# Performance work log

Hardware: AMD Instinct MI355X
Metric: run time of the kernel (lower is better)

Reference implementation:

```python
import jax, jax.numpy as jnp
import numpy as np

N = 4096        # nodes (atoms)
E = 65536       # edges (avg degree 16)
H = 128         # hidden_channels
R = 32          # num_rbf
MAX_Z = 128
CUTOFF_UPPER = 4.5
LN_EPS = 1e-5


def _linear_params(key, out_f, in_f, bias=True, scale=None):
    kw, kb = jax.random.split(key)
    s = scale if scale is not None else (1.0 / np.sqrt(in_f))
    W = jax.random.uniform(kw, (out_f, in_f), jnp.float32, -s, s)
    if bias:
        b = jax.random.uniform(kb, (out_f,), jnp.float32, -s, s)
        return W, b
    return W


def setup_inputs() -> dict:
    key = jax.random.key(0)
    ks = jax.random.split(key, 24)
    z = jax.random.randint(ks[0], (N,), 0, MAX_Z)
    edge_index = jax.random.randint(ks[1], (2, E), 0, N)
    edge_weight = jax.random.uniform(ks[2], (E,), jnp.float32) * CUTOFF_UPPER
    ev = jax.random.normal(ks[3], (E, 3), jnp.float32)
    edge_vec_norm = ev / jnp.linalg.norm(ev, axis=-1, keepdims=True)
    edge_attr = jax.random.uniform(ks[4], (E, R), jnp.float32)
    labels = jax.random.normal(ks[5], (N,), jnp.float32)
    labels_mask = jax.random.randint(ks[6], (N,), 0, 2).astype(bool)

    emb_w = jax.random.normal(ks[7], (MAX_Z, H), jnp.float32)  # nn.Embedding default N(0,1)
    emb2_w, emb2_b = _linear_params(ks[8], H, 2 * H)
    label_emb_w, label_emb_b = _linear_params(ks[9], H, 1)
    label_emb2_w, label_emb2_b = _linear_params(ks[10], H, 2 * H)
    mask_token = jax.random.normal(ks[11], (H,), jnp.float32)
    dp1_w, dp1_b = _linear_params(ks[12], H, R)
    dp2_w, dp2_b = _linear_params(ks[13], H, R)
    dp3_w, dp3_b = _linear_params(ks[14], H, R)
    lt0_w = _linear_params(ks[15], H, H, bias=False)
    lt1_w = _linear_params(ks[16], H, H, bias=False)
    lt2_w = _linear_params(ks[17], H, H, bias=False)
    ls1_w, ls1_b = _linear_params(ks[18], 2 * H, H)
    ls2_w, ls2_b = _linear_params(ks[19], 3 * H, 2 * H)
    ln_g = jnp.ones((H,), jnp.float32)
    ln_b = jnp.zeros((H,), jnp.float32)

    return dict(z=z, edge_index=edge_index, edge_weight=edge_weight,
                edge_vec_norm=edge_vec_norm, edge_attr=edge_attr,
                labels=labels, labels_mask=labels_mask,
                emb_w=emb_w, emb2_w=emb2_w, emb2_b=emb2_b,
                label_emb_w=label_emb_w, label_emb_b=label_emb_b,
                mask_token=mask_token,
                label_emb2_w=label_emb2_w, label_emb2_b=label_emb2_b,
                dp1_w=dp1_w, dp1_b=dp1_b, dp2_w=dp2_w, dp2_b=dp2_b,
                dp3_w=dp3_w, dp3_b=dp3_b,
                lt0_w=lt0_w, lt1_w=lt1_w, lt2_w=lt2_w,
                ls1_w=ls1_w, ls1_b=ls1_b, ls2_w=ls2_w, ls2_b=ls2_b,
                ln_g=ln_g, ln_b=ln_b)


def _cosine_cutoff(d):
    # cutoff_lower == 0 branch of CosineCutoff
    c = 0.5 * (jnp.cos(d * (np.pi / CUTOFF_UPPER)) + 1.0)
    return c * (d < CUTOFF_UPPER).astype(d.dtype)


def _skewtensor(v):
    zero = jnp.zeros_like(v[:, 0])
    t = jnp.stack([zero, -v[:, 2], v[:, 1],
                   v[:, 2], zero, -v[:, 0],
                   -v[:, 1], v[:, 0], zero], axis=1)
    return t.reshape(-1, 3, 3)


def _symtensor(v):
    vv = v[:, :, None] * v[:, None, :]               # [E,3,3], symmetric
    tr = jnp.trace(vv, axis1=-2, axis2=-1) / 3.0     # mean of diagonal
    eye = jnp.eye(3, dtype=v.dtype)
    return vv - tr[:, None, None] * eye              # traceless symmetric part


def _layernorm(x, g, b):
    mu = jnp.mean(x, axis=-1, keepdims=True)
    var = jnp.mean(jnp.square(x - mu), axis=-1, keepdims=True)
    return (x - mu) * jax.lax.rsqrt(var + LN_EPS) * g + b


def reference(z, edge_index, edge_weight, edge_vec_norm, edge_attr, labels,
              labels_mask, emb_w, emb2_w, emb2_b, label_emb_w, label_emb_b,
              mask_token, label_emb2_w, label_emb2_b, dp1_w, dp1_b, dp2_w,
              dp2_b, dp3_w, dp3_b, lt0_w, lt1_w, lt2_w, ls1_w, ls1_b, ls2_w,
              ls2_b, ln_g, ln_b):
    src, dst = edge_index[0], edge_index[1]
    n = z.shape[0]

    # --- atomic-number message: Zij = emb2(concat(Z[src], Z[dst])) ---
    Z = emb_w[z]                                                   # [N,H]
    Zij = jnp.concatenate([Z[src], Z[dst]], -1) @ emb2_w.T + emb2_b  # [E,H]

    # --- label message with mask-token substitution ---
    L = labels[:, None] @ label_emb_w.T + label_emb_b              # [N,H]
    L = jnp.where(labels_mask[:, None], mask_token, L)
    Lij = jnp.concatenate([L[src], L[dst]], -1) @ label_emb2_w.T + label_emb2_b

    # --- tensor messages ---
    CZ = _cosine_cutoff(edge_weight)[:, None] * (Zij + Lij)        # [E,H]
    eye = jnp.eye(3, dtype=edge_vec_norm.dtype)
    f1 = edge_attr @ dp1_w.T + dp1_b                               # [E,H]
    f2 = edge_attr @ dp2_w.T + dp2_b
    f3 = edge_attr @ dp3_w.T + dp3_b
    skew = _skewtensor(edge_vec_norm)                              # [E,3,3]
    sym = _symtensor(edge_vec_norm)                                # [E,3,3]
    Iij = (f1 * CZ)[:, :, None, None] * eye                        # [E,H,3,3]
    Aij = (f2 * CZ)[:, :, None, None] * skew[:, None]
    Sij = (f3 * CZ)[:, :, None, None] * sym[:, None]

    # --- scatter-add into node tensors ---
    I = jax.ops.segment_sum(Iij, src, num_segments=n)              # [N,H,3,3]
    A = jax.ops.segment_sum(Aij, src, num_segments=n)
    S = jax.ops.segment_sum(Sij, src, num_segments=n)

    # --- norm + scalar MLP gating ---
    X3 = I + A + S
    norm = jnp.sum(jnp.square(X3), axis=(-2, -1))                  # tensor_norm -> [N,H]
    norm = _layernorm(norm, ln_g, ln_b)
    norm = jax.nn.silu(norm @ ls1_w.T + ls1_b)                     # [N,2H]
    norm = jax.nn.silu(norm @ ls2_w.T + ls2_b)                     # [N,3H]
    norm = norm.reshape(n, -1, 3)                                  # [N,H,3]

    # --- channel-mixing linears over hidden dim, gated per component ---
    I = jnp.einsum('nhij,gh->ngij', I, lt0_w) * norm[:, :, 0, None, None]
    A = jnp.einsum('nhij,gh->ngij', A, lt1_w) * norm[:, :, 1, None, None]
    S = jnp.einsum('nhij,gh->ngij', S, lt2_w) * norm[:, :, 2, None, None]
    return I + A + S                                               # [N,H,3,3]
```

## Files before the change

### kernel.cpp

```cpp
#include <hip/hip_runtime.h>
#include <hip/hip_bf16.h>
#include <math.h>

#define NN 4096
#define EE 65536
#define HH 128
#define RR 32
#define MAXZ 128
#define CUT 4.5f
#define PI_OVER_CUT 0.6981317007977318f
#define LN_EPS 1e-5f

typedef unsigned short u16;
typedef unsigned int u32;
typedef unsigned char u8;
typedef _Float16 h2 __attribute__((ext_vector_type(2)));
typedef _Float16 hf8 __attribute__((ext_vector_type(8)));
typedef float f32x4 __attribute__((ext_vector_type(4)));

__device__ __forceinline__ float dot4(float4 a, float4 b){
    return a.x*b.x + a.y*b.y + a.z*b.z + a.w*b.w;
}
__device__ __forceinline__ float silu(float x){ return x / (1.f + __expf(-x)); }
__device__ __forceinline__ u32 packh2(float a, float b){
    union{u32 u; h2 h;} v; v.h = (h2){(_Float16)a, (_Float16)b}; return v.u;
}
__device__ __forceinline__ float fdot2u(u32 a, u32 b, float c){
    union{u32 u; h2 h;} x, y; x.u = a; y.u = b;
    return __builtin_amdgcn_fdot2(x.h, y.h, c, false);
}
__device__ __forceinline__ u16 f2h(float f){
    union{u16 u; _Float16 h;} v; v.h = (_Float16)f; return v.u;
}
__device__ __forceinline__ float h2f(u16 u){
    union{u16 u_; _Float16 h;} v; v.u_ = u; return (float)v.h;
}

__global__ void k_sig(float* __restrict__ out, float val, int n){
    int i = blockIdx.x*256 + threadIdx.x;
    if (i < n) out[i] = val;
}

__global__ void k_zero(int* __restrict__ deg){
    deg[blockIdx.x*256 + threadIdx.x] = 0;
}

__global__ __launch_bounds__(256) void k_cvt(const u8* __restrict__ zr,
                                             const u8* __restrict__ eir,
                                             const u8* __restrict__ mr,
                                             int* __restrict__ z32,
                                             int* __restrict__ ei32,
                                             int* __restrict__ m32,
                                             int* __restrict__ deg){
    __shared__ int sF1, sF3, sOdd, sZ64, sE64;
    int t = threadIdx.x;
    if (t == 0){ sF1=0; sF3=0; sOdd=0; sZ64=1; sE64=1; }
    __syncthreads();
    for (int i = t; i < 4096; i += 256){
        u8 b = mr[i];
        if ((i & 3) == 1 && b == 0x3F) sF1 = 1;
        if ((i & 3) == 3 && b == 0x3F) sF3 = 1;
        if ((i & 3) != 0 && b != 0)    sOdd = 1;
    }
    const u32* zw = (const u32*)zr;
    const u32* ew = (const u32*)eir;
    for (int i = t; i < 128; i += 256) if (zw[2*i + 1]) sZ64 = 0;
    for (int i = t; i < 512; i += 256) if (ew[2*i + 1]) sE64 = 0;
    __syncthreads();
    int mf = sF1 ? 2 : (sF3 ? 0 : (sOdd ? 1 : 0));
    int z64 = sZ64, e64 = sE64;

    int i = blockIdx.x*256 + t;
    if (i < NN){
        z32[i] = z64 ? ((const int*)zr)[2*i] : ((const int*)zr)[i];
        int mm;
        if (mf == 1)      mm = (mr[i] != 0);
        else if (mf == 2) mm = (((const u16*)mr)[i] != 0);
        else              mm = (((const u32*)mr)[i] != 0u);
        m32[i] = mm;
    }
    if (i < 2*EE){
        int v = e64 ? ((const int*)eir)[2*i] : ((const int*)eir)[i];
        ei32[i] = v;
        if (i < EE) atomicAdd(&deg[v], 1);
    }
}

__global__ __launch_bounds__(256) void k_scan(const int* __restrict__ deg,
                                              int* __restrict__ offsets,
                                              int* __restrict__ cursor){
    int t = threadIdx.x;
    int lane = t & 63, wid = t >> 6;
    int4 d[4];
    #pragma unroll
    for (int q = 0; q < 4; ++q) d[q] = ((const int4*)deg)[t*4 + q];
    int vals[16];
    #pragma unroll
    for (int q = 0; q < 4; ++q){
        vals[4*q+0]=d[q].x; vals[4*q+1]=d[q].y; vals[4*q+2]=d[q].z; vals[4*q+3]=d[q].w;
    }
    int sum = 0;
    #pragma unroll
    for (int q = 0; q < 16; ++q) sum += vals[q];
    int incl = sum;
    #pragma unroll
    for (int dd = 1; dd < 64; dd <<= 1){ int s = __shfl_up(incl, dd); if (lane >= dd) incl += s; }
    __shared__ int wsum[4];
    if (lane == 63) wsum[wid] = incl;
    __syncthreads();
    int base = 0;
    for (int w = 0; w < wid; ++w) base += wsum[w];
    int run = base + incl - sum;
    #pragma unroll
    for (int q = 0; q < 16; ++q){
        offsets[t*16 + q] = run;
        cursor [t*16 + q] = run;
        run += vals[q];
    }
    if (t == 255) offsets[NN] = run;
}

__global__ __launch_bounds__(256) void k_semeta(
    const int* __restrict__ ei, int* __restrict__ cursor,
    const float* __restrict__ ew, const float* __restrict__ ev,
    const float* __restrict__ ea,
    u32* __restrict__ attrSh, int* __restrict__ dstA, float4* __restrict__ metaA)
{
    int e = blockIdx.x*256 + threadIdx.x;
    if (e >= EE) return;
    int s = ei[e];
    int p = atomicAdd(&cursor[s], 1);
    float d = ew[e];
    float cutv = (d < CUT) ? 0.5f*(__cosf(d*PI_OVER_CUT) + 1.f) : 0.f;
    dstA[p] = ei[EE + e];
    metaA[p] = make_float4(cutv, ev[3*e], ev[3*e+1], ev[3*e+2]);
    const float* a = ea + (size_t)e*RR;
    u32* o = attrSh + (size_t)p*16;
    #pragma unroll
    for (int q = 0; q < 16; ++q)
        o[q] = packh2(cutv*a[2*q], cutv*a[2*q+1]);
}

__global__ __launch_bounds__(256) void k_prep(
    const float* __restrict__ ls1_w, const float* __restrict__ ls2_w,
    const float* __restrict__ lt0_w, const float* __restrict__ lt1_w,
    const float* __restrict__ lt2_w,
    const float* __restrict__ dp1_w, const float* __restrict__ dp2_w,
    const float* __restrict__ dp3_w,
    const float* __restrict__ emb_w, const float* __restrict__ emb2_w,
    const float* __restrict__ label_emb_w, const float* __restrict__ label_emb_b,
    const float* __restrict__ mask_token, const float* __restrict__ label_emb2_w,
    const float* __restrict__ label_emb2_b, const float* __restrict__ emb2_b,
    u16* __restrict__ ls1H, u16* __restrict__ ls2H, u16* __restrict__ ltH,
    u32* __restrict__ dpTh, float* __restrict__ PzA, float* __restrict__ PzB,
    float* __restrict__ vecs)
{
    int b = blockIdx.x, t = threadIdx.x;
    if (b < 728){
        int i = b*256 + t;
        if (i < 32768){ ls1H[i] = f2h(ls1_w[i]); return; }
        i -= 32768;
        if (i < 98304){ ls2H[i] = f2h(ls2_w[i]); return; }
        i -= 98304;
        if (i < 16384){ ltH[0*16384 + i] = f2h(lt0_w[i]); return; }
        i -= 16384;
        if (i < 16384){ ltH[1*16384 + i] = f2h(lt1_w[i]); return; }
        i -= 16384;
        if (i < 16384){ ltH[2*16384 + i] = f2h(lt2_w[i]); return; }
        i -= 16384;
        if (i < 6144){
            int j = i >> 11, rem = i & 2047, q = rem >> 7, h = rem & 127;
            const float* src = (j == 0) ? dp1_w : ((j == 1) ? dp2_w : dp3_w);
            dpTh[(j*16 + q)*HH + h] = packh2(src[h*RR + 2*q], src[h*RR + 2*q + 1]);
            return;
        }
        return;
    }
    if (b < 792){
        int zi = (b - 728)*2 + (t >> 7), h = t & 127;
        __shared__ float Zs[2][HH];
        Zs[t >> 7][h] = emb_w[zi*HH + h];
        __syncthreads();
        const float4* wa = (const float4*)(emb2_w + h*2*HH);
        const float4* wb = (const float4*)(emb2_w + h*2*HH + HH);
        float pa = 0.f, pb = 0.f;
        const float* Z = Zs[t >> 7];
        #pragma unroll 8
        for (int j = 0; j < HH/4; ++j){
            float4 zp = *(const float4*)&Z[4*j];
            pa += dot4(wa[j], zp);
            pb += dot4(wb[j], zp);
        }
        PzA[zi*HH + h] = pa;
        PzB[zi*HH + h] = pb;
        return;
    }
    if (t < 128){
        int h = t;
        const float* wa = label_emb2_w + h*2*HH;
        const float* wb = wa + HH;
        float uA=0.f,vA=0.f,wA=0.f,uB=0.f,vB=0.f,wB=0.f;
        for (int j = 0; j < HH; ++j){
            float a = wa[j], bb = wb[j];
            float u = label_emb_w[j], v = label_emb_b[j], m = mask_token[j];
            uA += a*u; vA += a*v; wA += a*m;
            uB += bb*u; vB += bb*v; wB += bb*m;
        }
        float bias = emb2_b[h] + label_emb2_b[h];
        vecs[0*HH + h] = uA;
        vecs[1*HH + h] = vA + bias;
        vecs[2*HH + h] = wA + bias;
        vecs[3*HH + h] = uB;
        vecs[4*HH + h] = vB;
        vecs[5*HH + h] = wB;
    }
}

__global__ __launch_bounds__(256) void k_comb(const int* __restrict__ z32,
                                              const int* __restrict__ m32,
                                              const float* __restrict__ labels,
                                              const float* __restrict__ PzA,
                                              const float* __restrict__ PzB,
                                              const float* __restrict__ vecs,
                                              float* __restrict__ Pa,
                                              u16* __restrict__ Pbh)
{
    int i = blockIdx.x*256 + threadIdx.x;
    int n = i >> 7, h = i & 127;
    int zi = z32[n];
    int mk = m32[n];
    float lab = labels[n];
    float la = mk ? vecs[2*HH + h] : lab*vecs[0*HH + h] + vecs[1*HH + h];
    float lb = mk ? vecs[5*HH + h] : lab*vecs[3*HH + h] + vecs[4*HH + h];
    Pa[i]  = PzA[zi*HH + h] + la;
    Pbh[i] = f2h(PzB[zi*HH + h] + lb);
}

__global__ __launch_bounds__(128) void k_gather(
    const u32* __restrict__ attrSh, const int* __restrict__ dstA,
    const float4* __restrict__ metaA,
    const u32* __restrict__ dpTh,
    const float* __restrict__ dp1_b, const float* __restrict__ dp2_b,
    const float* __restrict__ dp3_b,
    const float* __restrict__ Pa, const u16* __restrict__ Pbh,
    const int* __restrict__ offsets,
    u16* __restrict__ X0, u16* __restrict__ X1, u16* __restrict__ X2,
    float* __restrict__ norm2)
{
    int n = blockIdx.x, t = threadIdx.x;
    u32 w1[16], w2[16], w3[16];
    #pragma unroll
    for (int q = 0; q < 16; ++q){
        w1[q] = dpTh[(0*16 + q)*HH + t];
        w2[q] = dpTh[(1*16 + q)*HH + t];
        w3[q] = dpTh[(2*16 + q)*HH + t];
    }
    float fb1 = dp1_b[t], fb2 = dp2_b[t], fb3 = dp3_b[t];
    float pa = Pa[n*HH + t];
    float ai = 0.f, aw0 = 0.f, aw1 = 0.f, aw2 = 0.f;
    float m00 = 0.f, m01 = 0.f, m02 = 0.f, m11 = 0.f, m12 = 0.f, m22 = 0.f;

    int e0 = offsets[n], e1 = offsets[n+1];
    int j = e0;
    for (; j + 1 < e1; j += 2){
        int dsta = dstA[j], dstb = dstA[j+1];
        float4 ma = metaA[j], mb = metaA[j+1];
        float sa = pa + h2f(Pbh[(size_t)dsta*HH + t]);
        float sb = pa + h2f(Pbh[(size_t)dstb*HH + t]);
        const u32* Aa = attrSh + (size_t)j*16;
        const u32* Ab = Aa + 16;
        float f1a = ma.x*fb1, f2a = ma.x*fb2, f3a = ma.x*fb3;
        float f1b = mb.x*fb1, f2b = mb.x*fb2, f3b = mb.x*fb3;
        #pragma unroll
        for (int q = 0; q < 16; ++q){
            u32 a = Aa[q], bq = Ab[q];
            f1a = fdot2u(a, w1[q], f1a);
            f2a = fdot2u(a, w2[q], f2a);
            f3a = fdot2u(a, w3[q], f3a);
            f1b = fdot2u(bq, w1[q], f1b);
            f2b = fdot2u(bq, w2[q], f2b);
            f3b = fdot2u(bq, w3[q], f3b);
        }
        float aa = f1a*sa, ba = f2a*sa, ca = f3a*sa;
        float ab = f1b*sb, bb = f2b*sb, cb = f3b*sb;
        ai  += aa;            ai  += ab;
        aw0 += ba*ma.y;       aw0 += bb*mb.y;
        aw1 += ba*ma.z;       aw1 += bb*mb.z;
        aw2 += ba*ma.w;       aw2 += bb*mb.w;
        float cva0 = ca*ma.y, cva1 = ca*ma.z;
        float cvb0 = cb*mb.y, cvb1 = cb*mb.z;
        m00 += cva0*ma.y;     m00 += cvb0*mb.y;
        m01 += cva0*ma.z;     m01 += cvb0*mb.z;
        m02 += cva0*ma.w;     m02 += cvb0*mb.w;
        m11 += cva1*ma.z;     m11 += cvb1*mb.z;
        m12 += cva1*ma.w;     m12 += cvb1*mb.w;
        m22 += ca*ma.w*ma.w;  m22 += cb*mb.w*mb.w;
    }
    if (j < e1){
        int dst = dstA[j];
        float4 m4 = metaA[j];
        float s = pa + h2f(Pbh[(size_t)dst*HH + t]);
        const u32* Aa = attrSh + (size_t)j*16;
        float f1 = m4.x*fb1, f2 = m4.x*fb2, f3 = m4.x*fb3;
        #pragma unroll
        for (int q = 0; q < 16; ++q){
            u32 a = Aa[q];
            f1 = fdot2u(a, w1[q], f1);
            f2 = fdot2u(a, w2[q], f2);
            f3 = fdot2u(a, w3[q], f3);
        }
        float a = f1*s, b = f2*s, c = f3*s;
        ai  += a;
        aw0 += b*m4.y; aw1 += b*m4.z; aw2 += b*m4.w;
        float cv0 = c*m4.y, cv1 = c*m4.z;
        m00 += cv0*m4.y; m01 += cv0*m4.z; m02 += cv0*m4.w;
        m11 += cv1*m4.z; m12 += cv1*m4.w; m22 += c*m4.w*m4.w;
    }

    X0[(size_t)n*HH + t] = f2h(ai);
    u16* x1p = X1 + (size_t)3*n*HH + t;
    x1p[0*HH] = f2h(aw0); x1p[1*HH] = f2h(aw1); x1p[2*HH] = f2h(aw2);
    u16* x2p = X2 + (size_t)6*n*HH + t;
    x2p[0*HH] = f2h(m00); x2p[1*HH] = f2h(m01); x2p[2*HH] = f2h(m02);
    x2p[3*HH] = f2h(m11); x2p[4*HH] = f2h(m12); x2p[5*HH] = f2h(m22);

    float tr3 = (m00 + m11 + m22) * (1.f/3.f);
    float x00 = ai + m00 - tr3, x11 = ai + m11 - tr3, x22 = ai + m22 - tr3;
    float nn = x00*x00 + x11*x11 + x22*x22
             + 2.f*(m01*m01 + aw2*aw2 + m02*m02 + aw1*aw1 + m12*m12 + aw0*aw0);
    norm2[n*HH + t] = nn;
}

__global__ __launch_bounds__(256) void k_gatesM(
    const float* __restrict__ norm2, const float* __restrict__ ln_g,
    const float* __restrict__ ln_b,
    const u16* __restrict__ ls1H, const float* __restrict__ ls1_b,
    const u16* __restrict__ ls2H, const float* __restrict__ ls2_b,
    float* __restrict__ gates)
{
    int n0 = blockIdx.x * 16;
    int t = threadIdx.x;
    int wave = t >> 6, lane = t & 63;
    int rlo = lane & 15, kb = lane >> 4;
    __shared__ u16 ysH[16][136];
    __shared__ u16 usH[16][264];

    {
        int ni = wave*4 + kb;
        int n = n0 + ni;
        float x[8]; float s = 0.f;
        #pragma unroll
        for (int k = 0; k < 8; ++k){ x[k] = norm2[(size_t)n*HH + rlo + 16*k]; s += x[k]; }
        #pragma unroll
        for (int d = 1; d < 16; d <<= 1) s += __shfl_xor(s, d);
        float mu = s * (1.f/HH);
        float q = 0.f;
        #pragma unroll
        for (int k = 0; k < 8; ++k){ float dx = x[k]-mu; q += dx*dx; }
        #pragma unroll
        for (int d = 1; d < 16; d <<= 1) q += __shfl_xor(q, d);
        float rs = rsqrtf(q*(1.f/HH) + LN_EPS);
        #pragma unroll
        for (int k = 0; k < 8; ++k){
            int h = rlo + 16*k;
            ysH[ni][h] = f2h((x[k]-mu)*rs*ln_g[h] + ln_b[h]);
        }
    }
    __syncthreads();

    {
        hf8 a[4];
        #pragma unroll
        for (int ks = 0; ks < 4; ++ks)
            a[ks] = *(const hf8*)&ysH[rlo][kb*8 + ks*32];
        for (int ct = wave; ct < 16; ct += 4){
            f32x4 acc = (f32x4){0.f,0.f,0.f,0.f};
            const u16* wr0 = ls1H + (size_t)(ct*16 + rlo)*HH;
            #pragma unroll
            for (int ks = 0; ks < 4; ++ks){
                hf8 bf = *(const hf8*)(wr0 + kb*8 + ks*32);
                acc = __builtin_amdgcn_mfma_f32_16x16x32_f16(a[ks], bf, acc, 0, 0, 0);
            }
            float bias = ls1_b[ct*16 + rlo];
            #pragma unroll
            for (int j = 0; j < 4; ++j)
                usH[kb*4 + j][ct*16 + rlo] = f2h(silu(acc[j] + bias));
        }
    }
    __syncthreads();

    {
        hf8 a[8];
        #pragma unroll
        for (int ks = 0; ks < 8; ++ks)
            a[ks] = *(const hf8*)&usH[rlo][kb*8 + ks*32];
        for (int ct = wave; ct < 24; ct += 4){
            f32x4 acc = (f32x4){0.f,0.f,0.f,0.f};
            const u16* wr0 = ls2H + (size_t)(ct*16 + rlo)*256;
            #pragma unroll
            for (int ks = 0; ks < 8; ++ks){
                hf8 bf = *(const hf8*)(wr0 + kb*8 + ks*32);
                acc = __builtin_amdgcn_mfma_f32_16x16x32_f16(a[ks], bf, acc, 0, 0, 0);
            }
            float bias = ls2_b[ct*16 + rlo];
            #pragma unroll
            for (int j = 0; j < 4; ++j){
                int n = n0 + kb*4 + j;
                gates[(size_t)n*384 + ct*16 + rlo] = silu(acc[j] + bias);
            }
        }
    }
}

__global__ __launch_bounds__(256) void k_gemmout(
    const u16* __restrict__ X0, const u16* __restrict__ X1, const u16* __restrict__ X2,
    const u16* __restrict__ ltH, const float* __restrict__ gates,
    float* __restrict__ out)
{
    int n0 = blockIdx.x * 16;
    int wave = threadIdx.x >> 6, lane = threadIdx.x & 63;
    int rlo = lane & 15, kb = lane >> 4;
    __shared__ u16 Yl[160*136];

    for (int tile = wave; tile < 10; tile += 4){
        const u16* X; const u16* W; int rbase;
        if (tile == 0)     { X = X0; W = ltH;         rbase = n0; }
        else if (tile < 4) { X = X1; W = ltH + 16384; rbase = 3*n0 + (tile-1)*16; }
        else               { X = X2; W = ltH + 32768; rbase = 6*n0 + (tile-4)*16; }

        const hf8* xr = (const hf8*)(X + (size_t)(rbase + rlo)*HH + kb*8);
        hf8 a[4];
        #pragma unroll
        for (int ks = 0; ks < 4; ++ks) a[ks] = xr[ks*4];

        #pragma unroll
        for (int ct = 0; ct < 8; ++ct){
            f32x4 acc = (f32x4){0.f,0.f,0.f,0.f};
            const hf8* wr = (const hf8*)(W + (size_t)(ct*16 + rlo)*HH + kb*8);
            #pragma unroll
            for (int ks = 0; ks < 4; ++ks)
                acc = __builtin_amdgcn_mfma_f32_16x16x32_f16(a[ks], wr[ks*4], acc, 0, 0, 0);
            #pragma unroll
            for (int j = 0; j < 4; ++j)
                Yl[(tile*16 + kb*4 + j)*136 + ct*16 + rlo] = f2h(acc[j]);
        }
    }
    __syncthreads();

    #pragma unroll
    for (int q = 0; q < 8; ++q){
        int id = q*256 + threadIdx.x;
        int ni = id >> 7, g = id & 127;
        int n = n0 + ni;
        float mi  = h2f(Yl[ni*136 + g]);
        float mw0 = h2f(Yl[(16 + 3*ni + 0)*136 + g]);
        float mw1 = h2f(Yl[(16 + 3*ni + 1)*136 + g]);
        float mw2 = h2f(Yl[(16 + 3*ni + 2)*136 + g]);
        float mm0 = h2f(Yl[(64 + 6*ni + 0)*136 + g]);
        float mm1 = h2f(Yl[(64 + 6*ni + 1)*136 + g]);
        float mm2 = h2f(Yl[(64 + 6*ni + 2)*136 + g]);
        float mm3 = h2f(Yl[(64 + 6*ni + 3)*136 + g]);
        float mm4 = h2f(Yl[(64 + 6*ni + 4)*136 + g]);
        float mm5 = h2f(Yl[(64 + 6*ni + 5)*136 + g]);
        float g0 = gates[(size_t)n*384 + 3*g];
        float g1 = gates[(size_t)n*384 + 3*g + 1];
        float g2 = gates[(size_t)n*384 + 3*g + 2];
        float t3 = (mm0 + mm3 + mm5) * (1.f/3.f);
        float* op = out + ((size_t)n*HH + g)*9;
        op[0] =  g0*mi  + g2*(mm0 - t3);
        op[1] = -g1*mw2 + g2*mm1;
        op[2] =  g1*mw1 + g2*mm2;
        op[3] =  g1*mw2 + g2*mm1;
        op[4] =  g0*mi  + g2*(mm3 - t3);
        op[5] = -g1*mw0 + g2*mm4;
        op[6] = -g1*mw1 + g2*mm2;
        op[7] =  g1*mw0 + g2*mm4;
        op[8] =  g0*mi  + g2*(mm5 - t3);
    }
}

extern "C" void kernel_launch(void* const* d_in, const int* in_sizes, int n_in,
                              void* d_out, int out_size, void* d_ws, size_t ws_size,
                              hipStream_t stream)
{
    float* out = (float*)d_out;
    int sig_blocks = (out_size + 255)/256;

    if (out_size != NN*HH*9){
        k_sig<<<sig_blocks, 256, 0, stream>>>(out, 400.f, out_size);
        return;
    }
    if (n_in != 30){
        k_sig<<<sig_blocks, 256, 0, stream>>>(out, 300.f + (float)n_in, out_size);
        return;
    }
    static const int want[30] = {
        4096, 131072, 65536, 196608, 2097152, 4096, 4096,
        16384, 32768, 128, 128, 128, 128, 32768, 128,
        4096, 128, 4096, 128, 4096, 128,
        16384, 16384, 16384, 32768, 256, 98304, 384, 128, 128
    };
    for (int i = 0; i < 30; ++i){
        if (in_sizes[i] != want[i]){
            k_sig<<<sig_blocks, 256, 0, stream>>>(out, 200.f + (float)i, out_size);
            return;
        }
    }

    const u8*    z_raw        = (const u8*)d_in[0];
    const u8*    ei_raw       = (const u8*)d_in[1];
    const float* edge_weight  = (const float*)d_in[2];
    const float* edge_vec     = (const float*)d_in[3];
    const float* edge_attr    = (const float*)d_in[4];
    const float* labels       = (const float*)d_in[5];
    const u8*    mask_raw     = (const u8*)d_in[6];
    const float* emb_w        = (const float*)d_in[7];
    const float* emb2_w       = (const float*)d_in[8];
    const float* emb2_b       = (const float*)d_in[9];
    const float* label_emb_w  = (const float*)d_in[10];
    const float* label_emb_b  = (const float*)d_in[11];
    const float* mask_token   = (const float*)d_in[12];
    const float* label_emb2_w = (const float*)d_in[13];
    const float* label_emb2_b = (const float*)d_in[14];
    const float* dp1_w = (const float*)d_in[15];
    const float* dp1_b = (const float*)d_in[16];
    const float* dp2_w = (const float*)d_in[17];
    const float* dp2_b = (const float*)d_in[18];
    const float* dp3_w = (const float*)d_in[19];
    const float* dp3_b = (const float*)d_in[20];
    const float* lt0_w = (const float*)d_in[21];
    const float* lt1_w = (const float*)d_in[22];
    const float* lt2_w = (const float*)d_in[23];
    const float* ls1_w = (const float*)d_in[24];
    const float* ls1_b = (const float*)d_in[25];
    const float* ls2_w = (const float*)d_in[26];
    const float* ls2_b = (const float*)d_in[27];
    const float* ln_g  = (const float*)d_in[28];
    const float* ln_b  = (const float*)d_in[29];

    char* ws = (char*)d_ws;
    size_t off = 0;
    auto alloc = [&](size_t bytes) -> void* {
        void* p = ws + off;
        off += (bytes + 255) & ~(size_t)255;
        return p;
    };
    float* Pa      = (float*)alloc((size_t)NN*HH*4);
    u16*   Pbh     = (u16*)alloc((size_t)NN*HH*2);
    float* norm2   = (float*)alloc((size_t)NN*HH*4);
    float* gates   = (float*)alloc((size_t)NN*384*4);
    float* PzA     = (float*)alloc((size_t)MAXZ*HH*4);
    float* PzB     = (float*)alloc((size_t)MAXZ*HH*4);
    float* vecs    = (float*)alloc((size_t)6*HH*4);
    u32*   dpTh    = (u32*)alloc((size_t)3*16*HH*4);
    u16*   ls1H    = (u16*)alloc((size_t)32768*2);
    u16*   ls2H    = (u16*)alloc((size_t)98304*2);
    u16*   ltH     = (u16*)alloc((size_t)3*16384*2);
    u16*   X0      = (u16*)alloc((size_t)NN*HH*2);
    u16*   X1      = (u16*)alloc((size_t)3*NN*HH*2);
    u16*   X2      = (u16*)alloc((size_t)6*NN*HH*2);
    u32*   attrSh  = (u32*)alloc((size_t)EE*16*4);
    float* metaA   = (float*)alloc((size_t)EE*16);
    int*   dstA    = (int*)alloc((size_t)EE*4);
    int*   z32     = (int*)alloc((size_t)NN*4);
    int*   ei32    = (int*)alloc((size_t)2*EE*4);
    int*   m32     = (int*)alloc((size_t)NN*4);
    int*   deg     = (int*)alloc((size_t)NN*4);
    int*   offsets = (int*)alloc((size_t)(NN+1)*4);
    int*   cursor  = (int*)alloc((size_t)NN*4);

    if (off > ws_size){
        k_sig<<<sig_blocks, 256, 0, stream>>>(out, 150.f, out_size);
        return;
    }

    k_zero   <<<NN/256, 256, 0, stream>>>(deg);
    k_cvt    <<<(2*EE + 255)/256, 256, 0, stream>>>(z_raw, ei_raw, mask_raw,
                                                    z32, ei32, m32, deg);
    k_scan   <<<1, 256, 0, stream>>>(deg, offsets, cursor);
    k_semeta <<<EE/256, 256, 0, stream>>>(ei32, cursor, edge_weight, edge_vec,
                                          edge_attr, attrSh, dstA, (float4*)metaA);
    k_prep   <<<793, 256, 0, stream>>>(ls1_w, ls2_w, lt0_w, lt1_w, lt2_w,
                                       dp1_w, dp2_w, dp3_w,
                                       emb_w, emb2_w,
                                       label_emb_w, label_emb_b, mask_token,
                                       label_emb2_w, label_emb2_b, emb2_b,
                                       ls1H, ls2H, ltH, dpTh, PzA, PzB, vecs);
    k_comb   <<<NN*HH/256, 256, 0, stream>>>(z32, m32, labels, PzA, PzB, vecs, Pa, Pbh);
    k_gather <<<NN, 128, 0, stream>>>(attrSh, dstA, (const float4*)metaA,
                                      dpTh, dp1_b, dp2_b, dp3_b,
                                      Pa, Pbh, offsets, X0, X1, X2, norm2);
    k_gatesM <<<NN/16, 256, 0, stream>>>(norm2, ln_g, ln_b, ls1H, ls1_b,
                                         ls2H, ls2_b, gates);
    k_gemmout<<<256, 256, 0, stream>>>(X0, X1, X2, ltH, gates, out);
}
```

Baseline: 104.6 us.

## Merge front-end kernels with last-block scan, fuse edge/comb and gates/gemmout

Cuts the launch count from eight kernels to five. The convert, scan and weight-prep kernels become one launch, where the last block to finish (tracked by an atomic counter) runs the degree prefix scan. Edge sorting and node-embedding combination share one launch. The gates MLP and the output channel-mixing GEMM share a 512-thread block, with the X tiles prefetched before the MLP. The goal is less launch overhead and fewer idle gaps between small kernels, at the cost of a serialized last-block scan and higher per-block LDS and register use in the fused tail.

New measurement: 107.0 us. 1.02x slower.

```diff
diff --git a/kernel.cpp b/kernel.cpp
--- a/kernel.cpp
+++ b/kernel.cpp
@@ -41,107 +41,17 @@
     if (i < n) out[i] = val;
 }
 
-__global__ void k_zero(int* __restrict__ deg){
-    deg[blockIdx.x*256 + threadIdx.x] = 0;
-}
-
-__global__ __launch_bounds__(256) void k_cvt(const u8* __restrict__ zr,
-                                             const u8* __restrict__ eir,
-                                             const u8* __restrict__ mr,
-                                             int* __restrict__ z32,
-                                             int* __restrict__ ei32,
-                                             int* __restrict__ m32,
-                                             int* __restrict__ deg){
-    __shared__ int sF1, sF3, sOdd, sZ64, sE64;
-    int t = threadIdx.x;
-    if (t == 0){ sF1=0; sF3=0; sOdd=0; sZ64=1; sE64=1; }
-    __syncthreads();
-    for (int i = t; i < 4096; i += 256){
-        u8 b = mr[i];
-        if ((i & 3) == 1 && b == 0x3F) sF1 = 1;
-        if ((i & 3) == 3 && b == 0x3F) sF3 = 1;
-        if ((i & 3) != 0 && b != 0)    sOdd = 1;
-    }
-    const u32* zw = (const u32*)zr;
-    const u32* ew = (const u32*)eir;
-    for (int i = t; i < 128; i += 256) if (zw[2*i + 1]) sZ64 = 0;
-    for (int i = t; i < 512; i += 256) if (ew[2*i + 1]) sE64 = 0;
-    __syncthreads();
-    int mf = sF1 ? 2 : (sF3 ? 0 : (sOdd ? 1 : 0));
-    int z64 = sZ64, e64 = sE64;
-
-    int i = blockIdx.x*256 + t;
-    if (i < NN){
-        z32[i] = z64 ? ((const int*)zr)[2*i] : ((const int*)zr)[i];
-        int mm;
-        if (mf == 1)      mm = (mr[i] != 0);
-        else if (mf == 2) mm = (((const u16*)mr)[i] != 0);
-        else              mm = (((const u32*)mr)[i] != 0u);
-        m32[i] = mm;
-    }
-    if (i < 2*EE){
-        int v = e64 ? ((const int*)eir)[2*i] : ((const int*)eir)[i];
-        ei32[i] = v;
-        if (i < EE) atomicAdd(&deg[v], 1);
-    }
-}
-
-__global__ __launch_bounds__(256) void k_scan(const int* __restrict__ deg,
-                                              int* __restrict__ offsets,
-                                              int* __restrict__ cursor){
-    int t = threadIdx.x;
-    int lane = t & 63, wid = t >> 6;
-    int4 d[4];
-    #pragma unroll
-    for (int q = 0; q < 4; ++q) d[q] = ((const int4*)deg)[t*4 + q];
-    int vals[16];
-    #pragma unroll
-    for (int q = 0; q < 4; ++q){
-        vals[4*q+0]=d[q].x; vals[4*q+1]=d[q].y; vals[4*q+2]=d[q].z; vals[4*q+3]=d[q].w;
-    }
-    int sum = 0;
-    #pragma unroll
-    for (int q = 0; q < 16; ++q) sum += vals[q];
-    int incl = sum;
-    #pragma unroll
-    for (int dd = 1; dd < 64; dd <<= 1){ int s = __shfl_up(incl, dd); if (lane >= dd) incl += s; }
-    __shared__ int wsum[4];
-    if (lane == 63) wsum[wid] = incl;
-    __syncthreads();
-    int base = 0;
-    for (int w = 0; w < wid; ++w) base += wsum[w];
-    int run = base + incl - sum;
-    #pragma unroll
-    for (int q = 0; q < 16; ++q){
-        offsets[t*16 + q] = run;
-        cursor [t*16 + q] = run;
-        run += vals[q];
-    }
-    if (t == 255) offsets[NN] = run;
-}
-
-__global__ __launch_bounds__(256) void k_semeta(
-    const int* __restrict__ ei, int* __restrict__ cursor,
-    const float* __restrict__ ew, const float* __restrict__ ev,
-    const float* __restrict__ ea,
-    u32* __restrict__ attrSh, int* __restrict__ dstA, float4* __restrict__ metaA)
-{
-    int e = blockIdx.x*256 + threadIdx.x;
-    if (e >= EE) return;
-    int s = ei[e];
-    int p = atomicAdd(&cursor[s], 1);
-    float d = ew[e];
-    float cutv = (d < CUT) ? 0.5f*(__cosf(d*PI_OVER_CUT) + 1.f) : 0.f;
-    dstA[p] = ei[EE + e];
-    metaA[p] = make_float4(cutv, ev[3*e], ev[3*e+1], ev[3*e+2]);
-    const float* a = ea + (size_t)e*RR;
-    u32* o = attrSh + (size_t)p*16;
-    #pragma unroll
-    for (int q = 0; q < 16; ++q)
-        o[q] = packh2(cutv*a[2*q], cutv*a[2*q+1]);
-}
-
-__global__ __launch_bounds__(256) void k_prep(
+__global__ void k_zero(int* __restrict__ deg, int* __restrict__ doneCnt){
+    int i = blockIdx.x*256 + threadIdx.x;
+    deg[i] = 0;
+    if (i == 0) doneCnt[0] = 0;
+}
+
+__global__ __launch_bounds__(256) void k_front(
+    const u8* __restrict__ zr, const u8* __restrict__ eir, const u8* __restrict__ mr,
+    int* __restrict__ z32, int* __restrict__ ei32, int* __restrict__ m32,
+    int* __restrict__ deg, int* __restrict__ doneCnt,
+    int* __restrict__ offsets, int* __restrict__ cursor,
     const float* __restrict__ ls1_w, const float* __restrict__ ls2_w,
     const float* __restrict__ lt0_w, const float* __restrict__ lt1_w,
     const float* __restrict__ lt2_w,
@@ -156,8 +66,84 @@
     float* __restrict__ vecs)
 {
     int b = blockIdx.x, t = threadIdx.x;
-    if (b < 728){
+    if (b < 512){
+        __shared__ int sF1, sF3, sOdd, sZ64, sE64;
+        if (t == 0){ sF1=0; sF3=0; sOdd=0; sZ64=1; sE64=1; }
+        __syncthreads();
+        for (int i = t; i < 4096; i += 256){
+            u8 bb = mr[i];
+            if ((i & 3) == 1 && bb == 0x3F) sF1 = 1;
+            if ((i & 3) == 3 && bb == 0x3F) sF3 = 1;
+            if ((i & 3) != 0 && bb != 0)    sOdd = 1;
+        }
+        const u32* zw = (const u32*)zr;
+        const u32* ew = (const u32*)eir;
+        for (int i = t; i < 128; i += 256) if (zw[2*i + 1]) sZ64 = 0;
+        for (int i = t; i < 512; i += 256) if (ew[2*i + 1]) sE64 = 0;
+        __syncthreads();
+        int mf = sF1 ? 2 : (sF3 ? 0 : (sOdd ? 1 : 0));
+        int z64 = sZ64, e64 = sE64;
+
         int i = b*256 + t;
+        if (i < NN){
+            z32[i] = z64 ? ((const int*)zr)[2*i] : ((const int*)zr)[i];
+            int mm;
+            if (mf == 1)      mm = (mr[i] != 0);
+            else if (mf == 2) mm = (((const u16*)mr)[i] != 0);
+            else              mm = (((const u32*)mr)[i] != 0u);
+            m32[i] = mm;
+        }
+        if (i < 2*EE){
+            int v = e64 ? ((const int*)eir)[2*i] : ((const int*)eir)[i];
+            ei32[i] = v;
+            if (i < EE) atomicAdd(&deg[v], 1);
+        }
+
+        __syncthreads();
+        __shared__ int isLast;
+        if (t == 0){
+            __threadfence();
+            int old = __hip_atomic_fetch_add(doneCnt, 1, __ATOMIC_ACQ_REL,
+                                             __HIP_MEMORY_SCOPE_AGENT);
+            isLast = (old == 511);
+        }
+        __syncthreads();
+        if (isLast){
+            int lane = t & 63, wid = t >> 6;
+            int vals[16];
+            #pragma unroll
+            for (int q = 0; q < 16; ++q)
+                vals[q] = __hip_atomic_load(&deg[t*16 + q], __ATOMIC_RELAXED,
+                                            __HIP_MEMORY_SCOPE_AGENT);
+            int sum = 0;
+            #pragma unroll
+            for (int q = 0; q < 16; ++q) sum += vals[q];
+            int incl = sum;
+            #pragma unroll
+            for (int dd = 1; dd < 64; dd <<= 1){
+                int s2 = __shfl_up(incl, dd);
+                if (lane >= dd) incl += s2;
+            }
+            __shared__ int wsum[4];
+            if (lane == 63) wsum[wid] = incl;
+            __syncthreads();
+            int base = 0;
+            for (int w = 0; w < wid; ++w) base += wsum[w];
+            int run = base + incl - sum;
+            #pragma unroll
+            for (int q = 0; q < 16; ++q){
+                offsets[t*16 + q] = run;
+                cursor [t*16 + q] = run;
+                run += vals[q];
+            }
+            if (t == 255) offsets[NN] = run;
+        }
+        return;
+    }
+
+    int pb = b - 512;
+    if (pb < 728){
+        int i = pb*256 + t;
         if (i < 32768){ ls1H[i] = f2h(ls1_w[i]); return; }
         i -= 32768;
         if (i < 98304){ ls2H[i] = f2h(ls2_w[i]); return; }
@@ -176,23 +162,23 @@
         }
         return;
     }
-    if (b < 792){
-        int zi = (b - 728)*2 + (t >> 7), h = t & 127;
+    if (pb < 792){
+        int zi = (pb - 728)*2 + (t >> 7), h = t & 127;
         __shared__ float Zs[2][HH];
         Zs[t >> 7][h] = emb_w[zi*HH + h];
         __syncthreads();
         const float4* wa = (const float4*)(emb2_w + h*2*HH);
         const float4* wb = (const float4*)(emb2_w + h*2*HH + HH);
-        float pa = 0.f, pb = 0.f;
+        float pa = 0.f, pbv = 0.f;
         const float* Z = Zs[t >> 7];
         #pragma unroll 8
         for (int j = 0; j < HH/4; ++j){
             float4 zp = *(const float4*)&Z[4*j];
-            pa += dot4(wa[j], zp);
-            pb += dot4(wb[j], zp);
+            pa  += dot4(wa[j], zp);
+            pbv += dot4(wb[j], zp);
         }
         PzA[zi*HH + h] = pa;
-        PzB[zi*HH + h] = pb;
+        PzB[zi*HH + h] = pbv;
         return;
     }
     if (t < 128){
@@ -216,16 +202,34 @@
     }
 }
 
-__global__ __launch_bounds__(256) void k_comb(const int* __restrict__ z32,
-                                              const int* __restrict__ m32,
-                                              const float* __restrict__ labels,
-                                              const float* __restrict__ PzA,
-                                              const float* __restrict__ PzB,
-                                              const float* __restrict__ vecs,
-                                              float* __restrict__ Pa,
-                                              u16* __restrict__ Pbh)
+__global__ __launch_bounds__(256) void k_edge(
+    const int* __restrict__ ei, int* __restrict__ cursor,
+    const float* __restrict__ ew, const float* __restrict__ ev,
+    const float* __restrict__ ea,
+    u32* __restrict__ attrSh, int* __restrict__ dstA, float4* __restrict__ metaA,
+    const int* __restrict__ z32, const int* __restrict__ m32,
+    const float* __restrict__ labels,
+    const float* __restrict__ PzA, const float* __restrict__ PzB,
+    const float* __restrict__ vecs,
+    float* __restrict__ Pa, u16* __restrict__ Pbh)
 {
-    int i = blockIdx.x*256 + threadIdx.x;
+    int b = blockIdx.x, t = threadIdx.x;
+    if (b < 256){
+        int e = b*256 + t;
+        int s = ei[e];
+        int p = atomicAdd(&cursor[s], 1);
+        float d = ew[e];
+        float cutv = (d < CUT) ? 0.5f*(__cosf(d*PI_OVER_CUT) + 1.f) : 0.f;
+        dstA[p] = ei[EE + e];
+        metaA[p] = make_float4(cutv, ev[3*e], ev[3*e+1], ev[3*e+2]);
+        const float* a = ea + (size_t)e*RR;
+        u32* o = attrSh + (size_t)p*16;
+        #pragma unroll
+        for (int q = 0; q < 16; ++q)
+            o[q] = packh2(cutv*a[2*q], cutv*a[2*q+1]);
+        return;
+    }
+    int i = (b - 256)*256 + t;
     int n = i >> 7, h = i & 127;
     int zi = z32[n];
     int mk = m32[n];
@@ -309,9 +313,9 @@
             f2 = fdot2u(a, w2[q], f2);
             f3 = fdot2u(a, w3[q], f3);
         }
-        float a = f1*s, b = f2*s, c = f3*s;
+        float a = f1*s, bb = f2*s, c = f3*s;
         ai  += a;
-        aw0 += b*m4.y; aw1 += b*m4.z; aw2 += b*m4.w;
+        aw0 += bb*m4.y; aw1 += bb*m4.z; aw2 += bb*m4.w;
         float cv0 = c*m4.y, cv1 = c*m4.z;
         m00 += cv0*m4.y; m01 += cv0*m4.z; m02 += cv0*m4.w;
         m11 += cv1*m4.z; m12 += cv1*m4.w; m22 += c*m4.w*m4.w;
@@ -331,12 +335,15 @@
     norm2[n*HH + t] = nn;
 }
 
-__global__ __launch_bounds__(256) void k_gatesM(
+__global__ __launch_bounds__(512) void k_tail(
     const float* __restrict__ norm2, const float* __restrict__ ln_g,
     const float* __restrict__ ln_b,
     const u16* __restrict__ ls1H, const float* __restrict__ ls1_b,
     const u16* __restrict__ ls2H, const float* __restrict__ ls2_b,
-    float* __restrict__ gates)
+    float* __restrict__ gates,
+    const u16* __restrict__ X0, const u16* __restrict__ X1,
+    const u16* __restrict__ X2, const u16* __restrict__ ltH,
+    float* __restrict__ out)
 {
     int n0 = blockIdx.x * 16;
     int t = threadIdx.x;
@@ -344,8 +351,28 @@
     int rlo = lane & 15, kb = lane >> 4;
     __shared__ u16 ysH[16][136];
     __shared__ u16 usH[16][264];
-
+    __shared__ u16 Yl[160*136];
+
+    hf8 a0[4], a1[4];
     {
+        int tile = wave;
+        const u16* X; int rbase;
+        if (tile == 0)     { X = X0; rbase = n0; }
+        else if (tile < 4) { X = X1; rbase = 3*n0 + (tile-1)*16; }
+        else               { X = X2; rbase = 6*n0 + (tile-4)*16; }
+        const hf8* xr = (const hf8*)(X + (size_t)(rbase + rlo)*HH + kb*8);
+        #pragma unroll
+        for (int ks = 0; ks < 4; ++ks) a0[ks] = xr[ks*4];
+    }
+    if (wave < 2){
+        int tile = wave + 8;
+        int rbase = 6*n0 + (tile-4)*16;
+        const hf8* xr = (const hf8*)(X2 + (size_t)(rbase + rlo)*HH + kb*8);
+        #pragma unroll
+        for (int ks = 0; ks < 4; ++ks) a1[ks] = xr[ks*4];
+    }
+
+    if (wave < 4){
         int ni = wave*4 + kb;
         int n = n0 + ni;
         float x[8]; float s = 0.f;
@@ -373,7 +400,7 @@
         #pragma unroll
         for (int ks = 0; ks < 4; ++ks)
             a[ks] = *(const hf8*)&ysH[rlo][kb*8 + ks*32];
-        for (int ct = wave; ct < 16; ct += 4){
+        for (int ct = wave; ct < 16; ct += 8){
             f32x4 acc = (f32x4){0.f,0.f,0.f,0.f};
             const u16* wr0 = ls1H + (size_t)(ct*16 + rlo)*HH;
             #pragma unroll
@@ -394,7 +421,7 @@
         #pragma unroll
         for (int ks = 0; ks < 8; ++ks)
             a[ks] = *(const hf8*)&usH[rlo][kb*8 + ks*32];
-        for (int ct = wave; ct < 24; ct += 4){
+        for (int ct = wave; ct < 24; ct += 8){
             f32x4 acc = (f32x4){0.f,0.f,0.f,0.f};
             const u16* wr0 = ls2H + (size_t)(ct*16 + rlo)*256;
             #pragma unroll
@@ -410,46 +437,42 @@
             }
         }
     }
-}
-
-__global__ __launch_bounds__(256) void k_gemmout(
-    const u16* __restrict__ X0, const u16* __restrict__ X1, const u16* __restrict__ X2,
-    const u16* __restrict__ ltH, const float* __restrict__ gates,
-    float* __restrict__ out)
-{
-    int n0 = blockIdx.x * 16;
-    int wave = threadIdx.x >> 6, lane = threadIdx.x & 63;
-    int rlo = lane & 15, kb = lane >> 4;
-    __shared__ u16 Yl[160*136];
-
-    for (int tile = wave; tile < 10; tile += 4){
-        const u16* X; const u16* W; int rbase;
-        if (tile == 0)     { X = X0; W = ltH;         rbase = n0; }
-        else if (tile < 4) { X = X1; W = ltH + 16384; rbase = 3*n0 + (tile-1)*16; }
-        else               { X = X2; W = ltH + 32768; rbase = 6*n0 + (tile-4)*16; }
-
-        const hf8* xr = (const hf8*)(X + (size_t)(rbase + rlo)*HH + kb*8);
-        hf8 a[4];
-        #pragma unroll
-        for (int ks = 0; ks < 4; ++ks) a[ks] = xr[ks*4];
-
+
+    {
+        int tile = wave;
+        const u16* W = (tile == 0) ? ltH : ((tile < 4) ? ltH + 16384 : ltH + 32768);
         #pragma unroll
         for (int ct = 0; ct < 8; ++ct){
             f32x4 acc = (f32x4){0.f,0.f,0.f,0.f};
             const hf8* wr = (const hf8*)(W + (size_t)(ct*16 + rlo)*HH + kb*8);
             #pragma unroll
             for (int ks = 0; ks < 4; ++ks)
-                acc = __builtin_amdgcn_mfma_f32_16x16x32_f16(a[ks], wr[ks*4], acc, 0, 0, 0);
+                acc = __builtin_amdgcn_mfma_f32_16x16x32_f16(a0[ks], wr[ks*4], acc, 0, 0, 0);
             #pragma unroll
             for (int j = 0; j < 4; ++j)
                 Yl[(tile*16 + kb*4 + j)*136 + ct*16 + rlo] = f2h(acc[j]);
         }
     }
+    if (wave < 2){
+        int tile = wave + 8;
+        const u16* W = ltH + 32768;
+        #pragma unroll
+        for (int ct = 0; ct < 8; ++ct){
+            f32x4 acc = (f32x4){0.f,0.f,0.f,0.f};
+            const hf8* wr = (const hf8*)(W + (size_t)(ct*16 + rlo)*HH + kb*8);
+            #pragma unroll
+            for (int ks = 0; ks < 4; ++ks)
+                acc = __builtin_amdgcn_mfma_f32_16x16x32_f16(a1[ks], wr[ks*4], acc, 0, 0, 0);
+            #pragma unroll
+            for (int j = 0; j < 4; ++j)
+                Yl[(tile*16 + kb*4 + j)*136 + ct*16 + rlo] = f2h(acc[j]);
+        }
+    }
     __syncthreads();
 
     #pragma unroll
-    for (int q = 0; q < 8; ++q){
-        int id = q*256 + threadIdx.x;
+    for (int q = 0; q < 4; ++q){
+        int id = q*512 + t;
         int ni = id >> 7, g = id & 127;
         int n = n0 + ni;
         float mi  = h2f(Yl[ni*136 + g]);
@@ -568,29 +591,30 @@
     int*   deg     = (int*)alloc((size_t)NN*4);
     int*   offsets = (int*)alloc((size_t)(NN+1)*4);
     int*   cursor  = (int*)alloc((size_t)NN*4);
+    int*   doneCnt = (int*)alloc((size_t)4);
 
     if (off > ws_size){
         k_sig<<<sig_blocks, 256, 0, stream>>>(out, 150.f, out_size);
         return;
     }
 
-    k_zero   <<<NN/256, 256, 0, stream>>>(deg);
-    k_cvt    <<<(2*EE + 255)/256, 256, 0, stream>>>(z_raw, ei_raw, mask_raw,
-                                                    z32, ei32, m32, deg);
-    k_scan   <<<1, 256, 0, stream>>>(deg, offsets, cursor);
-    k_semeta <<<EE/256, 256, 0, stream>>>(ei32, cursor, edge_weight, edge_vec,
-                                          edge_attr, attrSh, dstA, (float4*)metaA);
-    k_prep   <<<793, 256, 0, stream>>>(ls1_w, ls2_w, lt0_w, lt1_w, lt2_w,
+    k_zero  <<<NN/256, 256, 0, stream>>>(deg, doneCnt);
+    k_front <<<1305, 256, 0, stream>>>(z_raw, ei_raw, mask_raw,
+                                       z32, ei32, m32, deg, doneCnt,
+                                       offsets, cursor,
+                                       ls1_w, ls2_w, lt0_w, lt1_w, lt2_w,
                                        dp1_w, dp2_w, dp3_w,
                                        emb_w, emb2_w,
                                        label_emb_w, label_emb_b, mask_token,
                                        label_emb2_w, label_emb2_b, emb2_b,
                                        ls1H, ls2H, ltH, dpTh, PzA, PzB, vecs);
-    k_comb   <<<NN*HH/256, 256, 0, stream>>>(z32, m32, labels, PzA, PzB, vecs, Pa, Pbh);
-    k_gather <<<NN, 128, 0, stream>>>(attrSh, dstA, (const float4*)metaA,
-                                      dpTh, dp1_b, dp2_b, dp3_b,
-                                      Pa, Pbh, offsets, X0, X1, X2, norm2);
-    k_gatesM <<<NN/16, 256, 0, stream>>>(norm2, ln_g, ln_b, ls1H, ls1_b,
-                                         ls2H, ls2_b, gates);
-    k_gemmout<<<256, 256, 0, stream>>>(X0, X1, X2, ltH, gates, out);
-}
+    k_edge  <<<2304, 256, 0, stream>>>(ei32, cursor, edge_weight, edge_vec,
+                                       edge_attr, attrSh, dstA, (float4*)metaA,
+                                       z32, m32, labels, PzA, PzB, vecs, Pa, Pbh);
+    k_gather<<<NN, 128, 0, stream>>>(attrSh, dstA, (const float4*)metaA,
+                                     dpTh, dp1_b, dp2_b, dp3_b,
+                                     Pa, Pbh, offsets, X0, X1, X2, norm2);
+    k_tail  <<<NN/16, 512, 0, stream>>>(norm2, ln_g, ln_b, ls1H, ls1_b,
+                                        ls2H, ls2_b, gates,
+                                        X0, X1, X2, ltH, out);
+}
```

## Fuse gate MLP and output channel-mixing GEMM into one 512-thread kernel

Applied to the files above, without the earlier changes.

Merges k_gatesM and k_gemmout into a single k_tail kernel with 512 threads per 16-node block. The X0/X1/X2 tile loads are issued up front so they overlap the layernorm and gate MLP work. The gate GEMMs are spread across 8 waves, and the 10 output GEMM tiles are covered in one pass instead of striding. This removes one launch and the gap between kernels, and gates are consumed inside the same block. In exchange, each block needs about 57 KB of LDS, which may limit occupancy.

Result: faster. 101.3 us (-3.1%).

```diff
diff --git a/kernel.cpp b/kernel.cpp
--- a/kernel.cpp
+++ b/kernel.cpp
@@ -331,12 +331,15 @@
     norm2[n*HH + t] = nn;
 }
 
-__global__ __launch_bounds__(256) void k_gatesM(
+__global__ __launch_bounds__(512) void k_tail(
     const float* __restrict__ norm2, const float* __restrict__ ln_g,
     const float* __restrict__ ln_b,
     const u16* __restrict__ ls1H, const float* __restrict__ ls1_b,
     const u16* __restrict__ ls2H, const float* __restrict__ ls2_b,
-    float* __restrict__ gates)
+    float* __restrict__ gates,
+    const u16* __restrict__ X0, const u16* __restrict__ X1,
+    const u16* __restrict__ X2, const u16* __restrict__ ltH,
+    float* __restrict__ out)
 {
     int n0 = blockIdx.x * 16;
     int t = threadIdx.x;
@@ -344,8 +347,28 @@
     int rlo = lane & 15, kb = lane >> 4;
     __shared__ u16 ysH[16][136];
     __shared__ u16 usH[16][264];
-
+    __shared__ u16 Yl[160*136];
+
+    hf8 a0[4], a1[4];
     {
+        int tile = wave;
+        const u16* X; int rbase;
+        if (tile == 0)     { X = X0; rbase = n0; }
+        else if (tile < 4) { X = X1; rbase = 3*n0 + (tile-1)*16; }
+        else               { X = X2; rbase = 6*n0 + (tile-4)*16; }
+        const hf8* xr = (const hf8*)(X + (size_t)(rbase + rlo)*HH + kb*8);
+        #pragma unroll
+        for (int ks = 0; ks < 4; ++ks) a0[ks] = xr[ks*4];
+    }
+    if (wave < 2){
+        int tile = wave + 8;
+        int rbase = 6*n0 + (tile-4)*16;
+        const hf8* xr = (const hf8*)(X2 + (size_t)(rbase + rlo)*HH + kb*8);
+        #pragma unroll
+        for (int ks = 0; ks < 4; ++ks) a1[ks] = xr[ks*4];
+    }
+
+    if (wave < 4){
         int ni = wave*4 + kb;
         int n = n0 + ni;
         float x[8]; float s = 0.f;
@@ -373,7 +396,7 @@
         #pragma unroll
         for (int ks = 0; ks < 4; ++ks)
             a[ks] = *(const hf8*)&ysH[rlo][kb*8 + ks*32];
-        for (int ct = wave; ct < 16; ct += 4){
+        for (int ct = wave; ct < 16; ct += 8){
             f32x4 acc = (f32x4){0.f,0.f,0.f,0.f};
             const u16* wr0 = ls1H + (size_t)(ct*16 + rlo)*HH;
             #pragma unroll
@@ -394,7 +417,7 @@
         #pragma unroll
         for (int ks = 0; ks < 8; ++ks)
             a[ks] = *(const hf8*)&usH[rlo][kb*8 + ks*32];
-        for (int ct = wave; ct < 24; ct += 4){
+        for (int ct = wave; ct < 24; ct += 8){
             f32x4 acc = (f32x4){0.f,0.f,0.f,0.f};
             const u16* wr0 = ls2H + (size_t)(ct*16 + rlo)*256;
             #pragma unroll
@@ -410,46 +433,42 @@
             }
         }
     }
-}
-
-__global__ __launch_bounds__(256) void k_gemmout(
-    const u16* __restrict__ X0, const u16* __restrict__ X1, const u16* __restrict__ X2,
-    const u16* __restrict__ ltH, const float* __restrict__ gates,
-    float* __restrict__ out)
-{
-    int n0 = blockIdx.x * 16;
-    int wave = threadIdx.x >> 6, lane = threadIdx.x & 63;
-    int rlo = lane & 15, kb = lane >> 4;
-    __shared__ u16 Yl[160*136];
-
-    for (int tile = wave; tile < 10; tile += 4){
-        const u16* X; const u16* W; int rbase;
-        if (tile == 0)     { X = X0; W = ltH;         rbase = n0; }
-        else if (tile < 4) { X = X1; W = ltH + 16384; rbase = 3*n0 + (tile-1)*16; }
-        else               { X = X2; W = ltH + 32768; rbase = 6*n0 + (tile-4)*16; }
-
-        const hf8* xr = (const hf8*)(X + (size_t)(rbase + rlo)*HH + kb*8);
-        hf8 a[4];
-        #pragma unroll
-        for (int ks = 0; ks < 4; ++ks) a[ks] = xr[ks*4];
-
+
+    {
+        int tile = wave;
+        const u16* W = (tile == 0) ? ltH : ((tile < 4) ? ltH + 16384 : ltH + 32768);
         #pragma unroll
         for (int ct = 0; ct < 8; ++ct){
             f32x4 acc = (f32x4){0.f,0.f,0.f,0.f};
             const hf8* wr = (const hf8*)(W + (size_t)(ct*16 + rlo)*HH + kb*8);
             #pragma unroll
             for (int ks = 0; ks < 4; ++ks)
-                acc = __builtin_amdgcn_mfma_f32_16x16x32_f16(a[ks], wr[ks*4], acc, 0, 0, 0);
+                acc = __builtin_amdgcn_mfma_f32_16x16x32_f16(a0[ks], wr[ks*4], acc, 0, 0, 0);
             #pragma unroll
             for (int j = 0; j < 4; ++j)
                 Yl[(tile*16 + kb*4 + j)*136 + ct*16 + rlo] = f2h(acc[j]);
         }
     }
+    if (wave < 2){
+        int tile = wave + 8;
+        const u16* W = ltH + 32768;
+        #pragma unroll
+        for (int ct = 0; ct < 8; ++ct){
+            f32x4 acc = (f32x4){0.f,0.f,0.f,0.f};
+            const hf8* wr = (const hf8*)(W + (size_t)(ct*16 + rlo)*HH + kb*8);
+            #pragma unroll
+            for (int ks = 0; ks < 4; ++ks)
+                acc = __builtin_amdgcn_mfma_f32_16x16x32_f16(a1[ks], wr[ks*4], acc, 0, 0, 0);
+            #pragma unroll
+            for (int j = 0; j < 4; ++j)
+                Yl[(tile*16 + kb*4 + j)*136 + ct*16 + rlo] = f2h(acc[j]);
+        }
+    }
     __syncthreads();
 
     #pragma unroll
-    for (int q = 0; q < 8; ++q){
-        int id = q*256 + threadIdx.x;
+    for (int q = 0; q < 4; ++q){
+        int id = q*512 + t;
         int ni = id >> 7, g = id & 127;
         int n = n0 + ni;
         float mi  = h2f(Yl[ni*136 + g]);
@@ -590,7 +609,7 @@
     k_gather <<<NN, 128, 0, stream>>>(attrSh, dstA, (const float4*)metaA,
                                       dpTh, dp1_b, dp2_b, dp3_b,
                                       Pa, Pbh, offsets, X0, X1, X2, norm2);
-    k_gatesM <<<NN/16, 256, 0, stream>>>(norm2, ln_g, ln_b, ls1H, ls1_b,
-                                         ls2H, ls2_b, gates);
-    k_gemmout<<<256, 256, 0, stream>>>(X0, X1, X2, ltH, gates, out);
-}
+    k_tail   <<<NN/16, 512, 0, stream>>>(norm2, ln_g, ln_b, ls1H, ls1_b,
+                                         ls2H, ls2_b, gates,
+                                         X0, X1, X2, ltH, out);
+}
```
